# Kernel tuning notes

Hardware: AMD Instinct MI355X
Metric: run time of the kernel (lower is better)

Reference implementation:

```python
import jax, jax.numpy as jnp
import numpy as np

N = 150_000          # active BEV voxels
C = 128              # SHARED_CONV_CHANNEL
KK = 9               # 3x3 submanifold kernel
H = W = 1024         # BEV spatial shape at stride 8
OUT_CH = (3, 2, 1, 3, 2)   # hm, center, center_z, dim, rot
NH = 5
MAXO = 3
EPS = 1e-5
INIT_BIAS = -2.19


def _build_neighbor_idx():
    # Random sparse occupancy; pad index == N means 'inactive neighbor'
    rng = np.random.default_rng(0)
    flat = rng.choice(H * W, size=N, replace=False)
    ys, xs = flat // W, flat % W
    grid = np.full(H * W, N, dtype=np.int32)
    grid[flat] = np.arange(N, dtype=np.int32)
    nbr = np.full((N, KK), N, dtype=np.int32)
    k = 0
    for dy in (-1, 0, 1):
        for dx in (-1, 0, 1):
            ny, nx = ys + dy, xs + dx
            ok = (ny >= 0) & (ny < H) & (nx >= 0) & (nx < W)
            nbr[ok, k] = grid[(ny * W + nx)[ok]]
            k += 1
    return jnp.asarray(nbr)


def setup_inputs() -> dict:
    key = jax.random.key(0)
    k0, k1, k2 = jax.random.split(key, 3)
    x = jax.random.normal(k0, (N, C), jnp.float32)
    W1 = jax.random.normal(k1, (NH, KK, C, C), jnp.float32) * (2.0 / (KK * C)) ** 0.5  # kaiming
    gamma = jnp.ones((NH, C), jnp.float32)
    beta = jnp.zeros((NH, C), jnp.float32)
    W2 = jax.random.normal(k2, (NH, C, MAXO), jnp.float32) * 0.02
    b2 = jnp.zeros((NH, MAXO), jnp.float32).at[0, :OUT_CH[0]].set(INIT_BIAS)  # hm init_bias
    return {"x": x, "neighbor_idx": _build_neighbor_idx(),
            "W1": W1, "gamma": gamma, "beta": beta, "W2": W2, "b2": b2}


def reference(x, neighbor_idx, W1, gamma, beta, W2, b2):
    # pad row of zeros: inactive neighbors contribute nothing (submanifold conv)
    xp = jnp.concatenate([x, jnp.zeros((1, C), x.dtype)], axis=0)
    acc = jnp.zeros((NH, x.shape[0], C), x.dtype)
    for k in range(KK):                       # fixed 3x3 kernel loop
        g = xp[neighbor_idx[:, k]]            # [N, C] irregular gather
        acc = acc + jnp.einsum('nc,hcd->hnd', g, W1[:, k])
    # BatchNorm1d (training mode: batch stats over active voxels) + ReLU
    mean = acc.mean(axis=1, keepdims=True)
    var = ((acc - mean) ** 2).mean(axis=1, keepdims=True)
    h = (acc - mean) * jax.lax.rsqrt(var + EPS) * gamma[:, None, :] + beta[:, None, :]
    h = jax.nn.relu(h)
    # 1x1 SubMConv per head (padded to MAXO channels, masked)
    out = jnp.einsum('hnc,hco->hno', h, W2) + b2[:, None, :]   # [NH, N, MAXO]
    mask = (jnp.arange(MAXO)[None, :] < jnp.asarray(OUT_CH)[:, None]).astype(out.dtype)
    return out * mask[:, None, :]
```

## Files before the change

### kernel.cpp

```cpp
#include <hip/hip_runtime.h>

#define NPTS 150000
#define NHEAD 5
#define KTOT 1152
#define NTILES 1172
#define NBLK 586
#define HSTRIDE 592
#define EPSV 1e-5f
#define FXSCALE 1048576.0

typedef __bf16 bf16x8 __attribute__((ext_vector_type(8)));
typedef float f32x4 __attribute__((ext_vector_type(4)));
typedef unsigned short u16x8 __attribute__((ext_vector_type(8)));

#define WS_NEEDED 232509376UL

__device__ __forceinline__ unsigned short f2bf(float f) {
    unsigned int u = __float_as_uint(f);
    u += 0x7FFFu + ((u >> 16) & 1u);
    return (unsigned short)(u >> 16);
}

__device__ __forceinline__ void gload16(const void* g, void* l) {
    __builtin_amdgcn_global_load_lds((const __attribute__((address_space(1))) void*)g,
                                     (__attribute__((address_space(3))) void*)l, 16, 0, 0);
}

__global__ void k_pre(const float* __restrict__ x, unsigned short* __restrict__ xbf,
                      const float* __restrict__ W1, unsigned short* __restrict__ w1t,
                      const int* __restrict__ nbr, int* __restrict__ hist_t) {
    __shared__ int lh[512];
    const int bid = blockIdx.x;
    const int t = threadIdx.x;
    if (bid < 9376) {
        const size_t i8 = (size_t)bid * 256 + t;
        const size_t base = i8 * 8;
        if (base >= (size_t)(NPTS + 1) * 128) return;
        if (base < (size_t)NPTS * 128) {
            const f32x4 v0 = __builtin_nontemporal_load((const f32x4*)(x + base));
            const f32x4 v1 = __builtin_nontemporal_load((const f32x4*)(x + base + 4));
            u16x8 o;
            o[0] = f2bf(v0[0]); o[1] = f2bf(v0[1]); o[2] = f2bf(v0[2]); o[3] = f2bf(v0[3]);
            o[4] = f2bf(v1[0]); o[5] = f2bf(v1[1]); o[6] = f2bf(v1[2]); o[7] = f2bf(v1[3]);
            *(u16x8*)(xbf + base) = o;
        } else {
            u16x8 z = {0,0,0,0,0,0,0,0};
            *(u16x8*)(xbf + base) = z;
        }
    } else if (bid < 9376 + 2880) {
        const int idx = (bid - 9376) * 256 + t;
        const int d = idx & 127;
        const int c = (idx >> 7) & 127;
        const int hk = idx >> 14;
        const int k = hk % 9, h = hk / 9;
        const int col = h * 128 + d;
        const int p = k * 128 + c;
        const int s32 = p >> 5;
        const int j0 = (p >> 3) & 3;
        const int jj = j0 ^ ((col >> 1) & 3);
        w1t[(size_t)col * KTOT + s32 * 32 + jj * 8 + (p & 7)] = f2bf(W1[idx]);
    } else {
        const int b = bid - 12256;
        lh[t] = 0; lh[t + 256] = 0;
        __syncthreads();
        const int n = b * 256 + t;
        if (n < NPTS) {
            int pat = 0;
#pragma unroll
            for (int k = 0; k < 9; k++) pat |= (nbr[n * 9 + k] != NPTS) << k;
            atomicAdd(&lh[pat], 1);
        }
        __syncthreads();
        hist_t[t * HSTRIDE + b] = lh[t];
        hist_t[(t + 256) * HSTRIDE + b] = lh[t + 256];
    }
}

__global__ void k_scan1(int* __restrict__ hist_t, int* __restrict__ tot,
                        unsigned long long* __restrict__ sacc) {
    const int p = blockIdx.x;
    const int lane = threadIdx.x;
    if (lane == 0) {
        sacc[p] = 0ULL; sacc[512 + p] = 0ULL;
        if (p < 256) sacc[1024 + p] = 0ULL;
    }
    int run = 0;
    for (int c = 0; c < 10; c++) {
        const int i = c * 64 + lane;
        const int orig = (i < NBLK) ? hist_t[p * HSTRIDE + i] : 0;
        int v = orig;
        for (int d = 1; d < 64; d <<= 1) {
            const int w = __shfl_up(v, d);
            if (lane >= d) v += w;
        }
        if (i < NBLK) hist_t[p * HSTRIDE + i] = run + v - orig;
        run += __shfl(v, 63);
    }
    if (lane == 0) tot[p] = run;
}

__global__ __launch_bounds__(512) void k_scatter(
    const int* __restrict__ nbr, const int* __restrict__ hist_t,
    const int* __restrict__ tot, int* __restrict__ perm) {
    __shared__ int pat_s[256];
    __shared__ int bs[512];
    const int t = threadIdx.x, b = blockIdx.x;
    const int v0 = tot[t];
    bs[t] = v0;
    __syncthreads();
    for (int d = 1; d < 512; d <<= 1) {
        const int w = (t >= d) ? bs[t - d] : 0;
        __syncthreads();
        bs[t] += w;
        __syncthreads();
    }
    const int base_t = bs[t] - v0;
    __syncthreads();
    bs[t] = base_t;
    const int n = b * 256 + (t & 255);
    int pat = -1;
    if (t < 256) {
        if (n < NPTS) {
            pat = 0;
#pragma unroll
            for (int k = 0; k < 9; k++) pat |= (nbr[n * 9 + k] != NPTS) << k;
        }
        pat_s[t] = pat;
    }
    __syncthreads();
    if (t < 256 && n < NPTS) {
        int rank = 0;
        for (int j = 0; j < 256; j++) rank += (j < t) & (pat_s[j] == pat);
        perm[bs[pat] + hist_t[pat * HSTRIDE + b] + rank] = n;
    }
}

__global__ __launch_bounds__(512, 4) void k_gemm(
    const unsigned short* __restrict__ xbf,
    const unsigned short* __restrict__ w1t,
    const int* __restrict__ nbr,
    const int* __restrict__ perm,
    unsigned short* __restrict__ accw2,
    unsigned long long* __restrict__ sacc)
{
    __shared__ unsigned short ABC[28672];
    __shared__ int nbr_s[9 * 128];
    __shared__ int perm_s[128];
    __shared__ int mask_s;

    const int tid = threadIdx.x;
    const int wid = tid >> 6;
    const int lane = tid & 63;
    const int bm = blockIdx.x;
    const int b2 = blockIdx.y;
    const int tile = (bm * 331) % NTILES;
    const int tile0 = tile * 128;

    if (tid == 0) mask_s = 0;
    if (tid < 128) {
        const int gr = tile0 + tid;
        perm_s[tid] = (gr < NPTS) ? perm[gr] : NPTS;
    }
    __syncthreads();
    if (tid < 128) {
        const int prow = perm_s[tid];
        int pat = 0;
#pragma unroll
        for (int k = 0; k < 9; k++) {
            const int v = (prow < NPTS) ? nbr[prow * 9 + k] : NPTS;
            nbr_s[k * 128 + tid] = v;
            pat |= (v != NPTS) << k;
        }
        if (pat) atomicOr(&mask_s, pat);
    }
    __syncthreads();
    const int mask = mask_s | 16;
    const int steps = 4 * __builtin_popcount(mask);

    const int RM = (wid >> 2) * 64;
    const int CNl = (wid & 3) * 80;
    const int lr16 = lane >> 2;
    const int lb = lane & 3;
    const int jswS = (lb ^ ((lr16 >> 1) & 3)) * 8;

    f32x4 acc[4][5];
#pragma unroll
    for (int m = 0; m < 4; m++)
#pragma unroll
        for (int n = 0; n < 5; n++) acc[m][n] = f32x4{0.f, 0.f, 0.f, 0.f};

    auto stage = [&](int buf, int kn, int q) {
#pragma unroll
        for (int j = 0; j < 4; ++j) {
            const int g = wid + 8 * j;
            if (g < 8) {
                const int r = g * 16 + lr16;
                const int idx = nbr_s[kn * 128 + r];
                gload16(xbf + (size_t)idx * 128 + q * 32 + jswS,
                        (void*)(ABC + buf * 4096 + g * 512));
            } else if (g < 28) {
                const int gb = g - 8;
                const int lc = gb * 16 + lr16;
                gload16(w1t + (size_t)(b2 * 320 + lc) * KTOT + (kn * 4 + q) * 32 + lb * 8,
                        (void*)(ABC + 8192 + buf * 10240 + gb * 512));
            }
        }
    };

    const int rlo = lane & 15;
    const int jsw = (((lane >> 4) ^ ((rlo >> 1) & 3))) * 8;

    auto compute = [&](int buf) {
        const unsigned short* Ab = ABC + buf * 4096;
        const unsigned short* Bb = ABC + 8192 + buf * 10240;
        bf16x8 a[4];
#pragma unroll
        for (int m = 0; m < 4; m++)
            a[m] = *reinterpret_cast<const bf16x8*>(&Ab[(RM + m * 16 + rlo) * 32 + jsw]);
#pragma unroll
        for (int n = 0; n < 5; n++) {
            const bf16x8 b = *reinterpret_cast<const bf16x8*>(&Bb[(CNl + n * 16 + rlo) * 32 + jsw]);
#pragma unroll
            for (int m = 0; m < 4; m++)
                acc[m][n] = __builtin_amdgcn_mfma_f32_16x16x32_bf16(a[m], b, acc[m][n], 0, 0, 0);
        }
    };

    int ckn = __builtin_ctz(mask), cq = 0, rem = mask & (mask - 1), buf = 0;
    stage(0, ckn, 0);
    __syncthreads();
    for (int i = 0; i < steps; i++) {
        int nkn, nq, nrem;
        if (cq < 3) { nkn = ckn; nq = cq + 1; nrem = rem; }
        else { nkn = rem ? __builtin_ctz(rem) : 0; nq = 0; nrem = rem & (rem - 1); }
        if (i + 1 < steps) stage(buf ^ 1, nkn, nq);
        compute(buf);
        __syncthreads();
        ckn = nkn; cq = nq; rem = nrem; buf ^= 1;
    }

    float sn[5], qn[5];
#pragma unroll
    for (int n = 0; n < 5; n++) {
        float s = 0.f, q = 0.f;
#pragma unroll
        for (int m = 0; m < 4; m++)
#pragma unroll
            for (int r = 0; r < 4; r++) { const float v = acc[m][n][r]; s += v; q += v * v; }
        s += __shfl_xor(s, 16); s += __shfl_xor(s, 32);
        q += __shfl_xor(q, 16); q += __shfl_xor(q, 32);
        sn[n] = s; qn[n] = q;
    }
    if (lane < 16) {
#pragma unroll
        for (int n = 0; n < 5; n++) {
            const int gcol = b2 * 320 + CNl + n * 16 + lane;
            atomicAdd(&sacc[gcol],
                      (unsigned long long)__double2ll_rn((double)sn[n] * FXSCALE));
            atomicAdd(&sacc[640 + gcol],
                      (unsigned long long)__double2ll_rn((double)qn[n] * FXSCALE));
        }
    }

    unsigned short* C = (unsigned short*)ABC;
#pragma unroll
    for (int p = 0; p < 2; ++p) {
        __syncthreads();
        if (((wid >> 1) & 1) == p) {
            const int colbase = CNl - p * 160;
#pragma unroll
            for (int m = 0; m < 4; m++) {
                const int row = RM + m * 16 + (lane >> 4) * 4;
#pragma unroll
                for (int n = 0; n < 5; n++) {
                    const int col = colbase + n * 16 + rlo;
#pragma unroll
                    for (int r = 0; r < 4; r++)
                        C[(row + r) * 168 + col] = f2bf(acc[m][n][r]);
                }
            }
        }
        __syncthreads();
#pragma unroll
        for (int j = 0; j < 5; j++) {
            const int chunk = tid + 512 * j;
            const int row = chunk / 20, cc = chunk % 20;
            const int prow = perm_s[row];
            if (prow < NPTS) {
                const int col = b2 * 320 + p * 160 + cc * 8;
                __builtin_nontemporal_store(*(const u16x8*)&C[row * 168 + cc * 8],
                    (u16x8*)(accw2 + (size_t)prow * 640 + col));
            }
        }
    }
}

__global__ __launch_bounds__(512) void k_out(
    const unsigned short* __restrict__ accw2,
    const unsigned long long* __restrict__ sacc,
    const float* __restrict__ gamma, const float* __restrict__ beta,
    const float* __restrict__ W2, const float* __restrict__ b2,
    float* __restrict__ out)
{
    __shared__ float sc[640], sh[640], w2s[1920], b2s[15];
    __shared__ float red[128][4][6];
    const int t = threadIdx.x;
    for (int c = t; c < 640; c += 512) {
        const double s = (double)(long long)sacc[c] * (1.0 / FXSCALE);
        const double q = (double)(long long)sacc[640 + c] * (1.0 / FXSCALE);
        const double mean = s * (1.0 / NPTS);
        const double var = q * (1.0 / NPTS) - mean * mean;
        const float rstd = (float)(1.0 / sqrt(var + (double)EPSV));
        const float g = gamma[c];
        sc[c] = rstd * g;
        sh[c] = beta[c] - (float)mean * rstd * g;
        w2s[c * 3 + 0] = W2[c * 3 + 0];
        w2s[c * 3 + 1] = W2[c * 3 + 1];
        w2s[c * 3 + 2] = W2[c * 3 + 2];
    }
    if (t < 15) b2s[t] = b2[t];
    __syncthreads();

    const int row = t >> 2;
    const int seg = t & 3;
    const int n0 = blockIdx.x * 128 + row;
    const int ccb = 16 - seg * 4;
    float o0[3] = {0.f, 0.f, 0.f}, o1[3] = {0.f, 0.f, 0.f};
    if (n0 < NPTS) {
        const unsigned short* rp = accw2 + (size_t)n0 * 640 + seg * 160;
        for (int cc = 0; cc < ccb; cc++) {
            const u16x8 v = *(const u16x8*)(rp + cc * 8);
#pragma unroll
            for (int j = 0; j < 8; j++) {
                const int c = seg * 160 + cc * 8 + j;
                const float a = __uint_as_float(((unsigned int)v[j]) << 16);
                const float hc = fmaxf(fmaf(a, sc[c], sh[c]), 0.f);
                o0[0] = fmaf(hc, w2s[c * 3 + 0], o0[0]);
                o0[1] = fmaf(hc, w2s[c * 3 + 1], o0[1]);
                o0[2] = fmaf(hc, w2s[c * 3 + 2], o0[2]);
            }
        }
        for (int cc = ccb; cc < 20; cc++) {
            const u16x8 v = *(const u16x8*)(rp + cc * 8);
#pragma unroll
            for (int j = 0; j < 8; j++) {
                const int c = seg * 160 + cc * 8 + j;
                const float a = __uint_as_float(((unsigned int)v[j]) << 16);
                const float hc = fmaxf(fmaf(a, sc[c], sh[c]), 0.f);
                o1[0] = fmaf(hc, w2s[c * 3 + 0], o1[0]);
                o1[1] = fmaf(hc, w2s[c * 3 + 1], o1[1]);
                o1[2] = fmaf(hc, w2s[c * 3 + 2], o1[2]);
            }
        }
    }
    red[row][seg][0] = o0[0]; red[row][seg][1] = o0[1]; red[row][seg][2] = o0[2];
    red[row][seg][3] = o1[0]; red[row][seg][4] = o1[1]; red[row][seg][5] = o1[2];
    __syncthreads();

    for (int idx = t; idx < 640; idx += 512) {
        const int h = idx >> 7, rw = idx & 127;
        const int n = blockIdx.x * 128 + rw;
        if (n < NPTS) {
            float a0 = b2s[h * 3 + 0], a1 = b2s[h * 3 + 1], a2 = b2s[h * 3 + 2];
            if (h >= 1) { a0 += red[rw][h - 1][3]; a1 += red[rw][h - 1][4]; a2 += red[rw][h - 1][5]; }
            if (h <= 3) { a0 += red[rw][h][0]; a1 += red[rw][h][1]; a2 += red[rw][h][2]; }
            const int noc = (h == 2) ? 1 : ((h == 1 || h == 4) ? 2 : 3);
            const size_t ob = ((size_t)h * NPTS + n) * 3;
            out[ob + 0] = (noc > 0) ? a0 : 0.f;
            out[ob + 1] = (noc > 1) ? a1 : 0.f;
            out[ob + 2] = (noc > 2) ? a2 : 0.f;
        }
    }
}

__global__ void k_sentinel(float* __restrict__ out, int n) {
    const int i = blockIdx.x * 256 + threadIdx.x;
    if (i < n) out[i] = 12345.0f;
}

extern "C" void kernel_launch(void* const* d_in, const int* in_sizes, int n_in,
                              void* d_out, int out_size, void* d_ws, size_t ws_size,
                              hipStream_t stream) {
    const float* x     = (const float*)d_in[0];
    const int*   nbr   = (const int*)d_in[1];
    const float* W1    = (const float*)d_in[2];
    const float* gamma = (const float*)d_in[3];
    const float* beta  = (const float*)d_in[4];
    const float* W2    = (const float*)d_in[5];
    const float* b2    = (const float*)d_in[6];
    float* out = (float*)d_out;

    if (ws_size < WS_NEEDED) {
        k_sentinel<<<(out_size + 255) / 256, 256, 0, stream>>>(out, out_size);
        return;
    }

    char* ws = (char*)d_ws;
    unsigned short* xbf      = (unsigned short*)(ws);
    unsigned short* w1t      = (unsigned short*)(ws + 38404096);
    unsigned short* accw2    = (unsigned short*)(ws + 39878656);
    int*            hist_t   = (int*)(ws + 39878656);
    int*            tot      = (int*)(ws + 39878656 + 2097152);
    unsigned long long* sacc = (unsigned long long*)(ws + 231899136);
    int*            perm     = (int*)(ws + 231909376);

    k_pre<<<12842, 256, 0, stream>>>(x, xbf, W1, w1t, nbr, hist_t);
    k_scan1<<<512, 64, 0, stream>>>(hist_t, tot, sacc);
    k_scatter<<<NBLK, 512, 0, stream>>>(nbr, hist_t, tot, perm);
    k_gemm<<<dim3(NTILES, 2), 512, 0, stream>>>(xbf, w1t, nbr, perm, accw2, sacc);
    k_out<<<NTILES, 512, 0, stream>>>(accw2, sacc, gamma, beta, W2, b2, out);
}
```

Baseline: 356.4 us.

## Store GEMM output in permuted tile order and unpermute in output kernel

The GEMM epilogue now writes accw2 rows contiguously in tile (permuted) order instead of scattering each row to its original voxel index. The output kernel reads contiguous permuted rows and applies the permutation only when writing the small final output. It also pads the per-segment shared-memory scale, shift and W2 arrays, transposes the reduction buffer to reduce bank conflicts, and fully unrolls the channel loop. The intent is to replace scattered 16-byte row stores from the GEMM with sequential writes, at the cost of scattered 12-byte output writes.

```diff
diff --git a/kernel.cpp b/kernel.cpp
--- a/kernel.cpp
+++ b/kernel.cpp
@@ -285,25 +285,25 @@
         for (int j = 0; j < 5; j++) {
             const int chunk = tid + 512 * j;
             const int row = chunk / 20, cc = chunk % 20;
-            const int prow = perm_s[row];
-            if (prow < NPTS) {
-                const int col = b2 * 320 + p * 160 + cc * 8;
-                __builtin_nontemporal_store(*(const u16x8*)&C[row * 168 + cc * 8],
-                    (u16x8*)(accw2 + (size_t)prow * 640 + col));
-            }
+            const int gr = tile0 + row;
+            const int col = b2 * 320 + p * 160 + cc * 8;
+            __builtin_nontemporal_store(*(const u16x8*)&C[row * 168 + cc * 8],
+                (u16x8*)(accw2 + (size_t)gr * 640 + col));
         }
     }
 }
 
 __global__ __launch_bounds__(512) void k_out(
     const unsigned short* __restrict__ accw2,
+    const int* __restrict__ perm,
     const unsigned long long* __restrict__ sacc,
     const float* __restrict__ gamma, const float* __restrict__ beta,
     const float* __restrict__ W2, const float* __restrict__ b2,
     float* __restrict__ out)
 {
-    __shared__ float sc[640], sh[640], w2s[1920], b2s[15];
-    __shared__ float red[128][4][6];
+    __shared__ float scp[672], shp[672], w2sp[1952], b2s[15];
+    __shared__ float red[4][128][6];
+    __shared__ int op_s[128];
     const int t = threadIdx.x;
     for (int c = t; c < 640; c += 512) {
         const double s = (double)(long long)sacc[c] * (1.0 / FXSCALE);
@@ -312,58 +312,58 @@
         const double var = q * (1.0 / NPTS) - mean * mean;
         const float rstd = (float)(1.0 / sqrt(var + (double)EPSV));
         const float g = gamma[c];
-        sc[c] = rstd * g;
-        sh[c] = beta[c] - (float)mean * rstd * g;
-        w2s[c * 3 + 0] = W2[c * 3 + 0];
-        w2s[c * 3 + 1] = W2[c * 3 + 1];
-        w2s[c * 3 + 2] = W2[c * 3 + 2];
+        const int sg = c / 160, off = c % 160;
+        scp[sg * 168 + off] = rstd * g;
+        shp[sg * 168 + off] = beta[c] - (float)mean * rstd * g;
+        w2sp[sg * 488 + off * 3 + 0] = W2[c * 3 + 0];
+        w2sp[sg * 488 + off * 3 + 1] = W2[c * 3 + 1];
+        w2sp[sg * 488 + off * 3 + 2] = W2[c * 3 + 2];
     }
     if (t < 15) b2s[t] = b2[t];
+    if (t < 128) {
+        const int gr = blockIdx.x * 128 + t;
+        op_s[t] = (gr < NPTS) ? perm[gr] : -1;
+    }
     __syncthreads();
 
     const int row = t >> 2;
     const int seg = t & 3;
-    const int n0 = blockIdx.x * 128 + row;
+    const int gr = blockIdx.x * 128 + row;
     const int ccb = 16 - seg * 4;
     float o0[3] = {0.f, 0.f, 0.f}, o1[3] = {0.f, 0.f, 0.f};
-    if (n0 < NPTS) {
-        const unsigned short* rp = accw2 + (size_t)n0 * 640 + seg * 160;
-        for (int cc = 0; cc < ccb; cc++) {
+    if (op_s[row] >= 0) {
+        const unsigned short* rp = accw2 + (size_t)gr * 640 + seg * 160;
+        const float* scb = scp + seg * 168;
+        const float* shb = shp + seg * 168;
+        const float* w2b = w2sp + seg * 488;
+#pragma unroll
+        for (int cc = 0; cc < 20; cc++) {
             const u16x8 v = *(const u16x8*)(rp + cc * 8);
+            float t0 = 0.f, t1 = 0.f, t2 = 0.f;
 #pragma unroll
             for (int j = 0; j < 8; j++) {
-                const int c = seg * 160 + cc * 8 + j;
+                const int off = cc * 8 + j;
                 const float a = __uint_as_float(((unsigned int)v[j]) << 16);
-                const float hc = fmaxf(fmaf(a, sc[c], sh[c]), 0.f);
-                o0[0] = fmaf(hc, w2s[c * 3 + 0], o0[0]);
-                o0[1] = fmaf(hc, w2s[c * 3 + 1], o0[1]);
-                o0[2] = fmaf(hc, w2s[c * 3 + 2], o0[2]);
+                const float hc = fmaxf(fmaf(a, scb[off], shb[off]), 0.f);
+                t0 = fmaf(hc, w2b[off * 3 + 0], t0);
+                t1 = fmaf(hc, w2b[off * 3 + 1], t1);
+                t2 = fmaf(hc, w2b[off * 3 + 2], t2);
             }
-        }
-        for (int cc = ccb; cc < 20; cc++) {
-            const u16x8 v = *(const u16x8*)(rp + cc * 8);
-#pragma unroll
-            for (int j = 0; j < 8; j++) {
-                const int c = seg * 160 + cc * 8 + j;
-                const float a = __uint_as_float(((unsigned int)v[j]) << 16);
-                const float hc = fmaxf(fmaf(a, sc[c], sh[c]), 0.f);
-                o1[0] = fmaf(hc, w2s[c * 3 + 0], o1[0]);
-                o1[1] = fmaf(hc, w2s[c * 3 + 1], o1[1]);
-                o1[2] = fmaf(hc, w2s[c * 3 + 2], o1[2]);
-            }
-        }
-    }
-    red[row][seg][0] = o0[0]; red[row][seg][1] = o0[1]; red[row][seg][2] = o0[2];
-    red[row][seg][3] = o1[0]; red[row][seg][4] = o1[1]; red[row][seg][5] = o1[2];
+            if (cc < ccb) { o0[0] += t0; o0[1] += t1; o0[2] += t2; }
+            else          { o1[0] += t0; o1[1] += t1; o1[2] += t2; }
+        }
+    }
+    red[seg][row][0] = o0[0]; red[seg][row][1] = o0[1]; red[seg][row][2] = o0[2];
+    red[seg][row][3] = o1[0]; red[seg][row][4] = o1[1]; red[seg][row][5] = o1[2];
     __syncthreads();
 
     for (int idx = t; idx < 640; idx += 512) {
         const int h = idx >> 7, rw = idx & 127;
-        const int n = blockIdx.x * 128 + rw;
-        if (n < NPTS) {
+        const int n = op_s[rw];
+        if (n >= 0) {
             float a0 = b2s[h * 3 + 0], a1 = b2s[h * 3 + 1], a2 = b2s[h * 3 + 2];
-            if (h >= 1) { a0 += red[rw][h - 1][3]; a1 += red[rw][h - 1][4]; a2 += red[rw][h - 1][5]; }
-            if (h <= 3) { a0 += red[rw][h][0]; a1 += red[rw][h][1]; a2 += red[rw][h][2]; }
+            if (h >= 1) { a0 += red[h - 1][rw][3]; a1 += red[h - 1][rw][4]; a2 += red[h - 1][rw][5]; }
+            if (h <= 3) { a0 += red[h][rw][0]; a1 += red[h][rw][1]; a2 += red[h][rw][2]; }
             const int noc = (h == 2) ? 1 : ((h == 1 || h == 4) ? 2 : 3);
             const size_t ob = ((size_t)h * NPTS + n) * 3;
             out[ob + 0] = (noc > 0) ? a0 : 0.f;
@@ -408,5 +408,5 @@
     k_scan1<<<512, 64, 0, stream>>>(hist_t, tot, sacc);
     k_scatter<<<NBLK, 512, 0, stream>>>(nbr, hist_t, tot, perm);
     k_gemm<<<dim3(NTILES, 2), 512, 0, stream>>>(xbf, w1t, nbr, perm, accw2, sacc);
-    k_out<<<NTILES, 512, 0, stream>>>(accw2, sacc, gamma, beta, W2, b2, out);
-}
+    k_out<<<NTILES, 512, 0, stream>>>(accw2, perm, sacc, gamma, beta, W2, b2, out);
+}
```

New measurement: 305.2 us (median of 2 runs). 14.4% less time.
